# Kernel tuning notes

Measured on AMD Instinct MI355X. Metric: run time of the kernel, lower is better.

## Reference

```python
import jax, jax.numpy as jnp
import numpy as np

# dims: batch, tokens, model dim, heads, head_dim, context len, n_blocks, ffn dim
B, L, D, H, HD, S, NB, DFF = 1, 3072, 1024, 16, 64, 512, 2, 4096
T3, H3, W3 = 12, 16, 16  # latent video grid, T3*H3*W3 == L


def _ln(x):
    # LayerNorm, elementwise_affine=False, eps=1e-6
    m = jnp.mean(x, axis=-1, keepdims=True)
    v = jnp.mean(jnp.square(x - m), axis=-1, keepdims=True)
    return (x - m) * jax.lax.rsqrt(v + 1e-6)


def _rot_half(x):
    x1, x2 = jnp.split(x, 2, axis=-1)
    return jnp.concatenate([-x2, x1], axis=-1)


def _rope3d(head_dim, t, h, w):
    d = head_dim // 6
    def band(n):
        freqs = 1.0 / 10000.0 ** (np.arange(0, 2 * d, 2, dtype=np.float32) / (2 * d))
        return np.outer(np.arange(n, dtype=np.float32), freqs)  # [n, d]
    te, he, we = band(t), band(h), band(w)
    rope = np.zeros((t, h, w, head_dim), dtype=np.float32)
    rope[:, :, :, :d] = te[:, None, None, :]
    rope[:, :, :, d:2 * d] = he[None, :, None, :]
    rope[:, :, :, 2 * d:3 * d] = we[None, None, :, :]
    return jnp.asarray(rope.reshape(t * h * w, head_dim))


def _forward(x, timestep_emb, context_emb, rope_emb, adaW, adab, sqW, skW, svW,
             soW, sob, cqW, ckW, cvW, coW, cob, f1W, f1b, f2W, f2b):
    Bv, Lv, Dv = x.shape
    hd = rope_emb.shape[-1]
    nh = Dv // hd
    scale = hd ** -0.5
    cos = jnp.cos(rope_emb)[None, None]  # [1,1,L,hd]
    sin = jnp.sin(rope_emb)[None, None]

    def heads(y):  # [B,N,D] -> [B,H,N,hd]
        return y.reshape(Bv, -1, nh, hd).transpose(0, 2, 1, 3)

    def merge(y):  # [B,H,L,hd] -> [B,L,D]
        return y.transpose(0, 2, 1, 3).reshape(Bv, Lv, Dv)

    for i in range(adaW.shape[0]):
        mods = timestep_emb @ adaW[i].T + adab[i]  # [B, 6D]
        sh_msa, sc_msa, g_msa, sh_mlp, sc_mlp, g_mlp = jnp.split(mods, 6, axis=-1)
        # --- AdaLN + self-attention with RoPE ---
        hx = _ln(x) * (1.0 + sc_msa[:, None, :]) + sh_msa[:, None, :]
        q, k, v = heads(hx @ sqW[i].T), heads(hx @ skW[i].T), heads(hx @ svW[i].T)
        q = q * cos + _rot_half(q) * sin
        k = k * cos + _rot_half(k) * sin
        a = jax.nn.softmax(jnp.einsum('bhld,bhmd->bhlm', q, k) * scale, axis=-1)
        o = merge(jnp.einsum('bhlm,bhmd->bhld', a, v))
        x = x + g_msa[:, None, :] * (o @ soW[i].T + sob[i])
        # --- cross-attention (no gate, no modulation) ---
        hx = _ln(x)
        q = heads(hx @ cqW[i].T)
        k = heads(context_emb @ ckW[i].T)
        v = heads(context_emb @ cvW[i].T)
        a = jax.nn.softmax(jnp.einsum('bhld,bhsd->bhls', q, k) * scale, axis=-1)
        o = merge(jnp.einsum('bhls,bhsd->bhld', a, v))
        x = x + (o @ coW[i].T + cob[i])
        # --- AdaLN + MLP (exact GELU) ---
        hx = _ln(x) * (1.0 + sc_mlp[:, None, :]) + sh_mlp[:, None, :]
        hx = jax.nn.gelu(hx @ f1W[i].T + f1b[i], approximate=False)
        x = x + g_mlp[:, None, :] * (hx @ f2W[i].T + f2b[i])
    return x


def setup_inputs() -> dict:
    ks = jax.random.split(jax.random.key(0), 20)
    s = 0.02
    return {
        'x': jax.random.normal(ks[0], (B, L, D), jnp.float32),
        'timestep_emb': jax.random.normal(ks[1], (B, D), jnp.float32),
        'context_emb': jax.random.normal(ks[2], (B, S, D), jnp.float32),
        'rope_emb': _rope3d(HD, T3, H3, W3),
        'adaW': jax.random.normal(ks[3], (NB, 6 * D, D), jnp.float32) * s,
        'adab': jnp.zeros((NB, 6 * D), jnp.float32),
        'sqW': jax.random.normal(ks[4], (NB, D, D), jnp.float32) * s,
        'skW': jax.random.normal(ks[5], (NB, D, D), jnp.float32) * s,
        'svW': jax.random.normal(ks[6], (NB, D, D), jnp.float32) * s,
        'soW': jax.random.normal(ks[7], (NB, D, D), jnp.float32) * s,
        'sob': jnp.zeros((NB, D), jnp.float32),
        'cqW': jax.random.normal(ks[8], (NB, D, D), jnp.float32) * s,
        'ckW': jax.random.normal(ks[9], (NB, D, D), jnp.float32) * s,
        'cvW': jax.random.normal(ks[10], (NB, D, D), jnp.float32) * s,
        'coW': jax.random.normal(ks[11], (NB, D, D), jnp.float32) * s,
        'cob': jnp.zeros((NB, D), jnp.float32),
        'f1W': jax.random.normal(ks[12], (NB, DFF, D), jnp.float32) * s,
        'f1b': jnp.zeros((NB, DFF), jnp.float32),
        'f2W': jax.random.normal(ks[13], (NB, D, DFF), jnp.float32) * s,
        'f2b': jnp.zeros((NB, D), jnp.float32),
    }


def reference(x, timestep_emb, context_emb, rope_emb, adaW, adab, sqW, skW, svW,
              soW, sob, cqW, ckW, cvW, coW, cob, f1W, f1b, f2W, f2b):
    return _forward(x, timestep_emb, context_emb, rope_emb, adaW, adab, sqW, skW,
                    svW, soW, sob, cqW, ckW, cvW, coW, cob, f1W, f1b, f2W, f2b)
```

## Files before the change

### kernel.cpp

```cpp
#include <hip/hip_runtime.h>
#include <math.h>

typedef __attribute__((ext_vector_type(8))) short bf16x8;
typedef __attribute__((ext_vector_type(4))) float f32x4;
typedef unsigned short u16;
typedef unsigned int u32;

#define DEV static __device__ __forceinline__

typedef __attribute__((address_space(3))) u32 lds_u32;
typedef const __attribute__((address_space(1))) u32 glb_u32;

DEV void gload16(const void* g, void* l){
  __builtin_amdgcn_global_load_lds((glb_u32*)g, (lds_u32*)l, 16, 0, 0);
}

DEV u16 f2bf(float f){
  u32 u = __builtin_bit_cast(u32, f);
  u32 r = (u + 0x7fffu + ((u >> 16) & 1u)) >> 16;
  return (u16)r;
}
DEV float bf2f(u16 h){
  u32 u = ((u32)h) << 16;
  return __builtin_bit_cast(float, u);
}
DEV u32 cvtpk(float a, float b){
  u32 r;
  asm("v_cvt_pk_bf16_f32 %0, %1, %2" : "=v"(r) : "v"(a), "v"(b));
  return r;
}
DEV float gelu_exact(float x){ return 0.5f*x*(1.f+erff(x*0.70710678118654752f)); }

#define QSCALE 0.18033688f

DEV void xcd_remap(int &bx, int &by){
  int gx = gridDim.x, gy = gridDim.y;
  int n = gx*gy;
  if ((n & 7) == 0){
    int id = by*gx + bx;
    int q = n >> 3;
    int sid = (id & 7)*q + (id >> 3);
    bx = sid % gx;
    by = sid / gx;
  }
}

__global__ __launch_bounds__(256) void k_copy_f32(const float* __restrict__ in, float* __restrict__ out, int n4){
  int i = blockIdx.x*256 + threadIdx.x;
  if (i < n4) ((float4*)out)[i] = ((const float4*)in)[i];
}

__global__ __launch_bounds__(256) void k_cvt_bf16(const float* __restrict__ in, u16* __restrict__ out, int n4){
  int i = blockIdx.x*256 + threadIdx.x;
  if (i < n4){
    float4 v = ((const float4*)in)[i];
    ushort4 o;
    o.x = f2bf(v.x); o.y = f2bf(v.y); o.z = f2bf(v.z); o.w = f2bf(v.w);
    ((ushort4*)out)[i] = o;
  }
}

struct CvtArgs { const float4* s[16]; ushort4* d[16]; };
__global__ __launch_bounds__(256) void k_cvt_all(CvtArgs a){
  int i = blockIdx.x*256 + threadIdx.x;
  int seg = i >> 19;
  int off = i & 0x7FFFF;
  float4 v = a.s[seg][off];
  ushort4 o;
  o.x = f2bf(v.x); o.y = f2bf(v.y); o.z = f2bf(v.z); o.w = f2bf(v.w);
  a.d[seg][off] = o;
}

__global__ __launch_bounds__(256) void k_trig(const float* __restrict__ rope,
    float2* __restrict__ ctq, float2* __restrict__ ctk){
  int i = blockIdx.x*256 + threadIdx.x;
  int d = i & 63;
  float a = rope[i];
  float c = cosf(a), s = sinf(a);
  float sg = (d < 32) ? -s : s;
  ctk[i] = make_float2(c, sg);
  ctq[i] = make_float2(c*QSCALE, sg*QSCALE);
}

__global__ __launch_bounds__(256) void k_ada(const float* __restrict__ te,
    const float* __restrict__ adaW, const float* __restrict__ adab,
    float* __restrict__ mods){
  int row = blockIdx.x*4 + (threadIdx.x>>6);
  int lane = threadIdx.x & 63;
  const float* wr = adaW + (size_t)row*1024;
  float s = 0.f;
  #pragma unroll
  for (int j=0; j<4; j++){
    int c = lane*4 + j*256;
    float4 a = *(const float4*)(te + c);
    float4 b = *(const float4*)(wr + c);
    s += a.x*b.x + a.y*b.y + a.z*b.z + a.w*b.w;
  }
  #pragma unroll
  for (int off=32; off; off>>=1) s += __shfl_down(s, off);
  if (!lane) mods[row] = s + adab[row];
}

__global__ __launch_bounds__(256) void k_ln_mod(const float* __restrict__ x,
    const float* __restrict__ sh, const float* __restrict__ sc,
    u16* __restrict__ out){
  int row = blockIdx.x, t = threadIdx.x;
  const float* xr = x + (size_t)row*1024;
  float4 v = ((const float4*)xr)[t];
  float s  = v.x+v.y+v.z+v.w;
  float sq = v.x*v.x+v.y*v.y+v.z*v.z+v.w*v.w;
  #pragma unroll
  for (int off=32; off; off>>=1){ s += __shfl_down(s,off); sq += __shfl_down(sq,off); }
  __shared__ float red[8];
  int w = t>>6, lane = t&63;
  if (!lane){ red[w] = s; red[4+w] = sq; }
  __syncthreads();
  s  = red[0]+red[1]+red[2]+red[3];
  sq = red[4]+red[5]+red[6]+red[7];
  float mean = s*(1.f/1024.f);
  float var  = sq*(1.f/1024.f) - mean*mean;
  float rst  = rsqrtf(var + 1e-6f);
  float vv[4] = {v.x, v.y, v.z, v.w};
  ushort4 o;
  u16 ob[4];
  #pragma unroll
  for (int j=0;j<4;j++){
    int col = t*4+j;
    float y = (vv[j]-mean)*rst;
    if (sh) y = y*(1.f + sc[col]) + sh[col];
    ob[j] = f2bf(y);
  }
  o.x=ob[0]; o.y=ob[1]; o.z=ob[2]; o.w=ob[3];
  *(ushort4*)(out + (size_t)row*1024 + t*4) = o;
}

__global__ __launch_bounds__(256) void k_rope(u16* __restrict__ q, u16* __restrict__ k,
    const float* __restrict__ rope){
  int idx = blockIdx.x*256 + threadIdx.x;
  int d = idx & 31;
  int h = (idx >> 5) & 15;
  int p = idx >> 9;
  const float* rr = rope + (size_t)p*64;
  float a0 = rr[d], a1 = rr[d+32];
  float c0 = cosf(a0), s0 = sinf(a0);
  float c1 = cosf(a1), s1 = sinf(a1);
  size_t o = (size_t)p*1024 + h*64 + d;
  float q0 = bf2f(q[o]), q1 = bf2f(q[o+32]);
  q[o]    = f2bf((q0*c0 - q1*s0)*QSCALE);
  q[o+32] = f2bf((q1*c1 + q0*s1)*QSCALE);
  float k0 = bf2f(k[o]), k1 = bf2f(k[o+32]);
  k[o]    = f2bf(k0*c0 - k1*s0);
  k[o+32] = f2bf(k1*c1 + k0*s1);
}

DEV void gemm_loop(const u16* __restrict__ X, const u16* __restrict__ W,
                   int bm, int bn, int ld, int lenK, u16* As, u16* Bs, f32x4 acc[4][4])
{
  int t = threadIdx.x;
  int w = t>>6, lane = t&63;
  int wr = (w>>1)*64, wc = (w&1)*64;
  int fr = lane&15, g = lane>>4;
  int arow = lane>>2, acol = (lane&3)*8;
  const u16* xp = X + (size_t)(bm + w*32 + arow)*ld + acol;
  const u16* wp = W + (size_t)(bn + w*32 + arow)*ld + acol;
  int nk = lenK >> 5;
  {
    u16* a = As + w*1024; u16* b = Bs + w*1024;
    gload16(xp, a);             gload16(xp + (size_t)16*ld, a + 512);
    gload16(wp, b);             gload16(wp + (size_t)16*ld, b + 512);
  }
  for (int kt = 0; kt < nk; ++kt){
    __syncthreads();
    int cur = kt & 1;
    if (kt + 1 < nk){
      int nb = cur ^ 1;
      int k0 = (kt+1) << 5;
      u16* a = As + nb*4096 + w*1024; u16* b = Bs + nb*4096 + w*1024;
      gload16(xp + k0, a);        gload16(xp + k0 + (size_t)16*ld, a + 512);
      gload16(wp + k0, b);        gload16(wp + k0 + (size_t)16*ld, b + 512);
    }
    const u16* ab = As + cur*4096;
    const u16* bb = Bs + cur*4096;
    bf16x8 a[4], b[4];
    #pragma unroll
    for (int i=0;i<4;i++) a[i] = *(const bf16x8*)(ab + (wr+i*16+fr)*32 + g*8);
    #pragma unroll
    for (int i=0;i<4;i++) b[i] = *(const bf16x8*)(bb + (wc+i*16+fr)*32 + g*8);
    __builtin_amdgcn_s_setprio(1);
    #pragma unroll
    for (int i=0;i<4;i++)
      #pragma unroll
      for (int j=0;j<4;j++)
        acc[i][j] = __builtin_amdgcn_mfma_f32_16x16x32_bf16(a[i], b[j], acc[i][j], 0, 0, 0);
    __builtin_amdgcn_s_setprio(0);
  }
}

template<int EPI>
__global__ __launch_bounds__(256) void k_gemm_bf16(
    const u16* __restrict__ X, const u16* __restrict__ W,
    const float* __restrict__ bias,
    u16* __restrict__ Yout,
    const float* __restrict__ resin, float* __restrict__ resout,
    const float* __restrict__ gate,
    int M, int N, int K)
{
  __shared__ __align__(16) u16 As[2*128*32];
  __shared__ __align__(16) u16 Bs[2*128*32];
  int bx = blockIdx.x, by = blockIdx.y;
  xcd_remap(bx, by);
  int bm = bx*128, bn = by*128;
  f32x4 acc[4][4] = {};
  gemm_loop(X, W, bm, bn, K, K, As, Bs, acc);
  int lane = threadIdx.x & 63, w = threadIdx.x>>6;
  int wr = (w>>1)*64, wc = (w&1)*64;
  int fr = lane&15, g = lane>>4;
  #pragma unroll
  for (int i=0;i<4;i++){
    #pragma unroll
    for (int j=0;j<4;j++){
      int col = bn + wc + j*16 + fr;
      float bv = bias ? bias[col] : 0.f;
      #pragma unroll
      for (int r=0;r<4;r++){
        int row = bm + wr + i*16 + g*4 + r;
        float y = acc[i][j][r] + bv;
        if (EPI == 1){
          Yout[(size_t)row*N + col] = f2bf(gelu_exact(y));
        } else if (EPI == 2){
          float gt = gate ? gate[col] : 1.f;
          resout[(size_t)row*N + col] = resin[(size_t)row*N + col] + gt*y;
        } else {
          Yout[(size_t)row*N + col] = f2bf(y*QSCALE);
        }
      }
    }
  }
}

__global__ __launch_bounds__(256) void k_gemm_part(
    const u16* __restrict__ X, const u16* __restrict__ W,
    float* __restrict__ pp, int M, int N, int K, int Ks)
{
  __shared__ __align__(16) u16 As[2*128*32];
  __shared__ __align__(16) u16 Bs[2*128*32];
  int bx = blockIdx.x, by = blockIdx.y;
  xcd_remap(bx, by);
  int s = blockIdx.z;
  int bm = bx*128, bn = by*128;
  f32x4 acc[4][4] = {};
  gemm_loop(X + (size_t)s*Ks, W + (size_t)s*Ks, bm, bn, K, Ks, As, Bs, acc);
  float* out = pp + (size_t)s*M*N;
  int lane = threadIdx.x & 63, w = threadIdx.x>>6;
  int wr = (w>>1)*64, wc = (w&1)*64;
  int fr = lane&15, g = lane>>4;
  #pragma unroll
  for (int i=0;i<4;i++)
    #pragma unroll
    for (int j=0;j<4;j++){
      int col = bn + wc + j*16 + fr;
      #pragma unroll
      for (int r=0;r<4;r++){
        int row = bm + wr + i*16 + g*4 + r;
        out[(size_t)row*N + col] = acc[i][j][r];
      }
    }
}

template<int EPI>
__global__ __launch_bounds__(256) void k_reduce(
    const float* __restrict__ pp, int S, const float* __restrict__ bias,
    const float* __restrict__ resin, float* __restrict__ resout,
    const float* __restrict__ gate, u16* __restrict__ Ybf,
    int MN, int N)
{
  int idx = blockIdx.x*256 + threadIdx.x;
  int base = idx*4;
  if (base >= MN) return;
  float4 s4 = *(const float4*)(pp + base);
  for (int s=1; s<S; ++s){
    float4 t4 = *(const float4*)(pp + (size_t)s*MN + base);
    s4.x += t4.x; s4.y += t4.y; s4.z += t4.z; s4.w += t4.w;
  }
  int col = base & (N-1);
  float b0=0,b1=0,b2=0,b3=0;
  if (bias){ b0=bias[col]; b1=bias[col+1]; b2=bias[col+2]; b3=bias[col+3]; }
  if (EPI == 2){
    float g0=1,g1=1,g2=1,g3=1;
    if (gate){ g0=gate[col]; g1=gate[col+1]; g2=gate[col+2]; g3=gate[col+3]; }
    float4 rv = *(const float4*)(resin + base);
    float4 o;
    o.x = rv.x + g0*(s4.x+b0);
    o.y = rv.y + g1*(s4.y+b1);
    o.z = rv.z + g2*(s4.z+b2);
    o.w = rv.w + g3*(s4.w+b3);
    *(float4*)(resout + base) = o;
  } else {
    ushort4 o;
    o.x = f2bf((s4.x+b0)*QSCALE);
    o.y = f2bf((s4.y+b1)*QSCALE);
    o.z = f2bf((s4.z+b2)*QSCALE);
    o.w = f2bf((s4.w+b3)*QSCALE);
    *(ushort4*)(Ybf + base) = o;
  }
}

template<int MOD>
__global__ __launch_bounds__(256) void k_reduce_ln(
    const float* __restrict__ pp, int S, const float* __restrict__ bias,
    const float* __restrict__ resin, float* __restrict__ resout,
    const float* __restrict__ gate,
    const float* __restrict__ sh, const float* __restrict__ sc,
    u16* __restrict__ hx)
{
  int row = blockIdx.x, t = threadIdx.x;
  size_t base = (size_t)row*1024 + t*4;
  const size_t MN = (size_t)3072*1024;
  float4 s4 = *(const float4*)(pp + base);
  for (int s=1; s<S; ++s){
    float4 t4 = *(const float4*)(pp + (size_t)s*MN + base);
    s4.x += t4.x; s4.y += t4.y; s4.z += t4.z; s4.w += t4.w;
  }
  int col = t*4;
  float b0=0,b1=0,b2=0,b3=0;
  if (bias){ b0=bias[col]; b1=bias[col+1]; b2=bias[col+2]; b3=bias[col+3]; }
  float g0=1,g1=1,g2=1,g3=1;
  if (gate){ g0=gate[col]; g1=gate[col+1]; g2=gate[col+2]; g3=gate[col+3]; }
  float4 rv = *(const float4*)(resin + base);
  float y[4];
  y[0] = rv.x + g0*(s4.x+b0);
  y[1] = rv.y + g1*(s4.y+b1);
  y[2] = rv.z + g2*(s4.z+b2);
  y[3] = rv.w + g3*(s4.w+b3);
  float4 ov; ov.x=y[0]; ov.y=y[1]; ov.z=y[2]; ov.w=y[3];
  *(float4*)(resout + base) = ov;
  float s  = y[0]+y[1]+y[2]+y[3];
  float sq = y[0]*y[0]+y[1]*y[1]+y[2]*y[2]+y[3]*y[3];
  #pragma unroll
  for (int off=32; off; off>>=1){ s += __shfl_down(s,off); sq += __shfl_down(sq,off); }
  __shared__ float red[8];
  int w = t>>6, lane = t&63;
  if (!lane){ red[w] = s; red[4+w] = sq; }
  __syncthreads();
  s  = red[0]+red[1]+red[2]+red[3];
  sq = red[4]+red[5]+red[6]+red[7];
  float mean = s*(1.f/1024.f);
  float var  = sq*(1.f/1024.f) - mean*mean;
  float rst  = rsqrtf(var + 1e-6f);
  ushort4 o;
  u16 ob[4];
  #pragma unroll
  for (int j=0;j<4;j++){
    float yy = (y[j]-mean)*rst;
    if (MOD) yy = yy*(1.f + sc[col+j]) + sh[col+j];
    ob[j] = f2bf(yy);
  }
  o.x=ob[0]; o.y=ob[1]; o.z=ob[2]; o.w=ob[3];
  *(ushort4*)(hx + base) = o;
}

template<int MODE>
__global__ __launch_bounds__(256) void k_qkv(
    const u16* __restrict__ X,
    const u16* __restrict__ W0, const u16* __restrict__ W1, const u16* __restrict__ W2,
    u16* __restrict__ Y0, u16* __restrict__ Y1, u16* __restrict__ VT,
    const float2* __restrict__ ctq, const float2* __restrict__ ctk,
    int M, int ldvt)
{
  __shared__ __align__(16) u16 As[2*128*32];
  __shared__ __align__(16) u16 Bs[2*128*32];
  int bx = blockIdx.x, by = blockIdx.y;
  xcd_remap(bx, by);
  int bm = bx*128, bn = by*128;
  int sel = bn >> 10;
  int bnl = bn & 1023;
  const u16* W = (sel==0 ? W0 : (sel==1 ? W1 : W2));
  f32x4 acc[4][4] = {};
  gemm_loop(X, W, bm, bnl, 1024, 1024, As, Bs, acc);
  int lane = threadIdx.x & 63, w = threadIdx.x>>6;
  int wr = (w>>1)*64, wc = (w&1)*64;
  int fr = lane&15, g = lane>>4;
  if (sel < 2){
    u16* Y = (sel==0) ? Y0 : Y1;
    const float2* ct = (sel==0) ? ctq : ctk;
    #pragma unroll
    for (int i=0;i<4;i++)
      #pragma unroll
      for (int j=0;j<4;j++){
        int col = bnl + wc + j*16 + fr;
        int d = j*16 + fr;
        #pragma unroll
        for (int r=0;r<4;r++){
          int row = bm + wr + i*16 + g*4 + r;
          float2 cs = ct[row*64 + d];
          float yv = acc[i][j][r]*cs.x + acc[i][j^2][r]*cs.y;
          Y[(size_t)row*1024 + col] = f2bf(yv);
        }
      }
  } else {
    #pragma unroll
    for (int i=0;i<4;i++)
      #pragma unroll
      for (int j=0;j<4;j++){
        int col = bnl + wc + j*16 + fr;
        int row0 = bm + wr + i*16 + g*4;
        uint2 pk;
        pk.x = cvtpk(acc[i][j][0], acc[i][j][1]);
        pk.y = cvtpk(acc[i][j][2], acc[i][j][3]);
        *(uint2*)(VT + (size_t)col*ldvt + row0) = pk;
      }
  }
}

__global__ __launch_bounds__(256) void k_kv64(
    const u16* __restrict__ X,
    const u16* __restrict__ Wk, const u16* __restrict__ Wv,
    u16* __restrict__ Kout, u16* __restrict__ VTout, int ldvt)
{
  __shared__ __align__(16) u16 As[2*64*32];
  __shared__ __align__(16) u16 Bs[2*64*32];
  int bx = blockIdx.x, by = blockIdx.y;
  xcd_remap(bx, by);
  int bm = bx*64;
  int sel = by >> 4;
  int bnl = (by & 15)*64;
  const u16* W = sel ? Wv : Wk;
  int t = threadIdx.x, w = t>>6, lane = t&63;
  int wr = (w>>1)*32, wc = (w&1)*32;
  int fr = lane&15, g = lane>>4;
  f32x4 acc[2][2] = {};
  int arow = lane>>2, acol = (lane&3)*8;
  const u16* xp = X + (size_t)(bm + w*16 + arow)*1024 + acol;
  const u16* wp = W + (size_t)(bnl + w*16 + arow)*1024 + acol;
  {
    gload16(xp, As + w*512);
    gload16(wp, Bs + w*512);
  }
  for (int kt = 0; kt < 32; ++kt){
    __syncthreads();
    int cur = kt & 1;
    if (kt + 1 < 32){
      int nb = cur ^ 1;
      int k0 = (kt+1) << 5;
      gload16(xp + k0, As + nb*2048 + w*512);
      gload16(wp + k0, Bs + nb*2048 + w*512);
    }
    const u16* ab = As + cur*2048;
    const u16* bb = Bs + cur*2048;
    bf16x8 a[2], b[2];
    #pragma unroll
    for (int i=0;i<2;i++) a[i] = *(const bf16x8*)(ab + (wr+i*16+fr)*32 + g*8);
    #pragma unroll
    for (int i=0;i<2;i++) b[i] = *(const bf16x8*)(bb + (wc+i*16+fr)*32 + g*8);
    __builtin_amdgcn_s_setprio(1);
    #pragma unroll
    for (int i=0;i<2;i++)
      #pragma unroll
      for (int j=0;j<2;j++)
        acc[i][j] = __builtin_amdgcn_mfma_f32_16x16x32_bf16(a[i], b[j], acc[i][j], 0, 0, 0);
    __builtin_amdgcn_s_setprio(0);
  }
  #pragma unroll
  for (int i=0;i<2;i++)
    #pragma unroll
    for (int j=0;j<2;j++){
      int col = bnl + wc + j*16 + fr;
      if (sel == 0){
        #pragma unroll
        for (int r=0;r<4;r++){
          int row = bm + wr + i*16 + g*4 + r;
          Kout[(size_t)row*1024 + col] = f2bf(acc[i][j][r]);
        }
      } else {
        int row0 = bm + wr + i*16 + g*4;
        uint2 pk;
        pk.x = cvtpk(acc[i][j][0], acc[i][j][1]);
        pk.y = cvtpk(acc[i][j][2], acc[i][j][3]);
        *(uint2*)(VTout + (size_t)col*ldvt + row0) = pk;
      }
    }
}

template<int EPI>
__global__ __launch_bounds__(256) void k_gemm_f32(
    const u16* __restrict__ X, const float* __restrict__ W,
    const float* __restrict__ bias,
    u16* __restrict__ Yout,
    const float* __restrict__ resin, float* __restrict__ resout,
    const float* __restrict__ gate,
    int M, int N, int K)
{
  __shared__ __align__(16) u16 As[128][32];
  __shared__ __align__(16) u16 Bs[128][40];
  int bx = blockIdx.x, by = blockIdx.y;
  xcd_remap(bx, by);
  int bm = bx*128, bn = by*128;
  int t = threadIdx.x;
  int w = t>>6, lane = t&63;
  int wr = (w>>1)*64, wc = (w&1)*64;
  int fr = lane&15, g = lane>>4;
  f32x4 acc[4][4] = {};
  int arow = lane>>2, acol = (lane&3)*8;
  int srow = t>>2, scol = (t&3)*8;
  for (int k0=0; k0<K; k0+=32){
    #pragma unroll
    for (int inst=0; inst<2; ++inst){
      int r = w*32 + inst*16 + arow;
      gload16(X + (size_t)(bm+r)*K + k0 + acol, &As[w*32+inst*16][0]);
    }
    #pragma unroll
    for (int it=0; it<2; ++it){
      const float* wp = W + (size_t)(bn+srow+it*64)*K + k0 + scol;
      float4 f0 = *(const float4*)(wp);
      float4 f1 = *(const float4*)(wp+4);
      uint4 bw;
      bw.x = (u32)f2bf(f0.x) | ((u32)f2bf(f0.y)<<16);
      bw.y = (u32)f2bf(f0.z) | ((u32)f2bf(f0.w)<<16);
      bw.z = (u32)f2bf(f1.x) | ((u32)f2bf(f1.y)<<16);
      bw.w = (u32)f2bf(f1.z) | ((u32)f2bf(f1.w)<<16);
      *(uint4*)&Bs[srow+it*64][scol] = bw;
    }
    __syncthreads();
    bf16x8 a[4], b[4];
    #pragma unroll
    for (int i=0;i<4;i++) a[i] = *(const bf16x8*)&As[wr+i*16+fr][g*8];
    #pragma unroll
    for (int i=0;i<4;i++) b[i] = *(const bf16x8*)&Bs[wc+i*16+fr][g*8];
    #pragma unroll
    for (int i=0;i<4;i++)
      #pragma unroll
      for (int j=0;j<4;j++)
        acc[i][j] = __builtin_amdgcn_mfma_f32_16x16x32_bf16(a[i], b[j], acc[i][j], 0, 0, 0);
    __syncthreads();
  }
  #pragma unroll
  for (int i=0;i<4;i++){
    #pragma unroll
    for (int j=0;j<4;j++){
      int col = bn + wc + j*16 + fr;
      float bv = bias ? bias[col] : 0.f;
      #pragma unroll
      for (int r=0;r<4;r++){
        int row = bm + wr + i*16 + g*4 + r;
        float y = acc[i][j][r] + bv;
        if (EPI == 0){
          Yout[(size_t)row*N + col] = f2bf(y);
        } else if (EPI == 1){
          Yout[(size_t)row*N + col] = f2bf(gelu_exact(y));
        } else if (EPI == 2){
          float gt = gate ? gate[col] : 1.f;
          resout[(size_t)row*N + col] = resin[(size_t)row*N + col] + gt*y;
        } else if (EPI == 3){
          Yout[(size_t)col*M + row] = f2bf(y);
        } else {
          Yout[(size_t)row*N + col] = f2bf(y*QSCALE);
        }
      }
    }
  }
}

__global__ __launch_bounds__(256) void k_flash(
    const u16* __restrict__ Q, const u16* __restrict__ Kb, const u16* __restrict__ VT,
    u16* __restrict__ O, int Lkv)
{
  __shared__ __align__(16) u16 Ks[2*64*64];
  __shared__ __align__(16) u16 Vs[2*64*64];
  __shared__ __align__(16) u16 Ps[4][16][72];
  int bx = blockIdx.x, by = blockIdx.y;
  xcd_remap(bx, by);
  int h = by;
  int q0 = bx*64;
  int t = threadIdx.x, w = t>>6, lane = t&63;
  int fr = lane&15, g = lane>>4;
  const u16* qrow = Q + (size_t)(q0 + w*16 + fr)*1024 + h*64;
  bf16x8 aq0 = *(const bf16x8*)(qrow + g*8);
  bf16x8 aq1 = *(const bf16x8*)(qrow + 32 + g*8);
  f32x4 accO[4] = {};
  float l = 0.f;
  int slot = lane & 7, rop = lane >> 3;
  const u16* kbase = Kb + (size_t)h*64;
  const u16* vbase = VT + (size_t)h*64*Lkv;
  int nt = Lkv >> 6;
  auto stage = [&](int tt){
    int buf = tt & 1;
    int k0 = tt << 6;
    #pragma unroll
    for (int inst=0; inst<2; ++inst){
      int row = w*16 + inst*8 + rop;
      int ss = slot ^ (row & 7);
      gload16(kbase + (size_t)(k0+row)*1024 + ss*8, Ks + buf*4096 + row*64);
      gload16(vbase + (size_t)row*Lkv + k0 + ss*8, Vs + buf*4096 + row*64);
    }
  };
  stage(0);
  bf16x8 vp0[4], vp1[4];
  for (int tt=0; tt<nt; ++tt){
    __syncthreads();
    int cur = tt & 1;
    const u16* kc = Ks + cur*4096;
    const u16* vc = Vs + cur*4096;
    bf16x8 vn0[4], vn1[4];
    #pragma unroll
    for (int nd=0; nd<4; nd++){
      int rowV = nd*16 + fr;
      vn0[nd] = *(const bf16x8*)(vc + rowV*64 + ((g  ) ^ (rowV&7))*8);
      vn1[nd] = *(const bf16x8*)(vc + rowV*64 + ((4+g) ^ (rowV&7))*8);
    }
    bf16x8 ap0, ap1;
    if (tt > 0){
      ap0 = *(const bf16x8*)&Ps[w][fr][g*8];
      ap1 = *(const bf16x8*)&Ps[w][fr][32 + g*8];
    }
    if (tt+1 < nt) stage(tt+1);
    f32x4 st[4] = {};
    __builtin_amdgcn_s_setprio(1);
    #pragma unroll
    for (int kb=0;kb<4;kb++){
      int rowK = kb*16 + fr;
      bf16x8 b0 = *(const bf16x8*)(kc + rowK*64 + ((g  ) ^ (rowK&7))*8);
      bf16x8 b1 = *(const bf16x8*)(kc + rowK*64 + ((4+g) ^ (rowK&7))*8);
      st[kb] = __builtin_amdgcn_mfma_f32_16x16x32_bf16(b0, aq0, st[kb], 0,0,0);
      st[kb] = __builtin_amdgcn_mfma_f32_16x16x32_bf16(b1, aq1, st[kb], 0,0,0);
    }
    if (tt > 0){
      #pragma unroll
      for (int nd=0; nd<4; nd++){
        accO[nd] = __builtin_amdgcn_mfma_f32_16x16x32_bf16(ap0, vp0[nd], accO[nd], 0,0,0);
        accO[nd] = __builtin_amdgcn_mfma_f32_16x16x32_bf16(ap1, vp1[nd], accO[nd], 0,0,0);
      }
    }
    __builtin_amdgcn_s_setprio(0);
    float ts = 0.f;
    u32 pk[8];
    #pragma unroll
    for (int kb=0;kb<4;kb++){
      float p0 = exp2f(st[kb][0]);
      float p1 = exp2f(st[kb][1]);
      float p2 = exp2f(st[kb][2]);
      float p3 = exp2f(st[kb][3]);
      ts += (p0+p1)+(p2+p3);
      pk[kb*2]   = cvtpk(p0,p1);
      pk[kb*2+1] = cvtpk(p2,p3);
    }
    ts += __shfl_xor(ts, 16);
    ts += __shfl_xor(ts, 32);
    l += ts;
    #pragma unroll
    for (int kb=0;kb<4;kb++){
      uint2 pv; pv.x = pk[kb*2]; pv.y = pk[kb*2+1];
      *(uint2*)&Ps[w][fr][kb*16 + g*4] = pv;
    }
    #pragma unroll
    for (int nd=0; nd<4; nd++){ vp0[nd] = vn0[nd]; vp1[nd] = vn1[nd]; }
  }
  {
    bf16x8 ap0 = *(const bf16x8*)&Ps[w][fr][g*8];
    bf16x8 ap1 = *(const bf16x8*)&Ps[w][fr][32 + g*8];
    #pragma unroll
    for (int nd=0; nd<4; nd++){
      accO[nd] = __builtin_amdgcn_mfma_f32_16x16x32_bf16(ap0, vp0[nd], accO[nd], 0,0,0);
      accO[nd] = __builtin_amdgcn_mfma_f32_16x16x32_bf16(ap1, vp1[nd], accO[nd], 0,0,0);
    }
  }
  float rl = 1.f / l;
  #pragma unroll
  for (int r=0;r<4;r++){
    float rlq = __shfl(rl, g*4+r);
    int row = q0 + w*16 + g*4 + r;
    #pragma unroll
    for (int nd=0; nd<4; nd++)
      O[(size_t)row*1024 + h*64 + nd*16 + fr] = f2bf(accO[nd][r] * rlq);
  }
}

extern "C" void kernel_launch(void* const* d_in, const int* in_sizes, int n_in,
                              void* d_out, int out_size, void* d_ws, size_t ws_size,
                              hipStream_t stream){
  const float* x_in = (const float*)d_in[0];
  const float* te   = (const float*)d_in[1];
  const float* ctx  = (const float*)d_in[2];
  const float* rope = (const float*)d_in[3];
  const float* adaW = (const float*)d_in[4];
  const float* adab = (const float*)d_in[5];
  const float* sqW  = (const float*)d_in[6];
  const float* skW  = (const float*)d_in[7];
  const float* svW  = (const float*)d_in[8];
  const float* soW  = (const float*)d_in[9];
  const float* sob  = (const float*)d_in[10];
  const float* cqW  = (const float*)d_in[11];
  const float* ckW  = (const float*)d_in[12];
  const float* cvW  = (const float*)d_in[13];
  const float* coW  = (const float*)d_in[14];
  const float* cob  = (const float*)d_in[15];
  const float* f1W  = (const float*)d_in[16];
  const float* f1b  = (const float*)d_in[17];
  const float* f2W  = (const float*)d_in[18];
  const float* f2b  = (const float*)d_in[19];
  float* x = (float*)d_out;

  char* p = (char*)d_ws;
  size_t used = 0;
  auto alloc = [&](size_t bytes){
    void* r = (void*)(p + used);
    used += (bytes + 255) & ~(size_t)255;
    return r;
  };
  u16* hx   = (u16*)alloc((size_t)3072*1024*2);
  u16* qb   = (u16*)alloc((size_t)3072*1024*2);
  u16* kb   = (u16*)alloc((size_t)3072*1024*2);
  u16* vt   = (u16*)alloc((size_t)1024*3072*2);
  u16* ob   = (u16*)alloc((size_t)3072*1024*2);
  u16* mid  = (u16*)alloc((size_t)3072*4096*2);
  u16* ctxb = (u16*)alloc((size_t)512*1024*2);
  float* mods = (float*)alloc((size_t)2*6144*4);
  float2* ctq = (float2*)alloc((size_t)3072*64*8);
  float2* ctk = (float2*)alloc((size_t)3072*64*8);
  size_t base_used = used;
  const size_t NW_SMALL = (size_t)2*1024*1024;
  const size_t NW_BIG   = (size_t)2*4096*1024;
  size_t wbytes = (8*NW_SMALL + 2*NW_BIG)*2;
  bool pre = (base_used + wbytes + 4096) <= ws_size;

  u16 *sqWb=nullptr,*skWb=nullptr,*svWb=nullptr,*soWb=nullptr,
      *cqWb=nullptr,*ckWb=nullptr,*cvWb=nullptr,*coWb=nullptr,
      *f1Wb=nullptr,*f2Wb=nullptr;
  if (pre){
    sqWb=(u16*)alloc(NW_SMALL*2); skWb=(u16*)alloc(NW_SMALL*2);
    svWb=(u16*)alloc(NW_SMALL*2); soWb=(u16*)alloc(NW_SMALL*2);
    cqWb=(u16*)alloc(NW_SMALL*2); ckWb=(u16*)alloc(NW_SMALL*2);
    cvWb=(u16*)alloc(NW_SMALL*2); coWb=(u16*)alloc(NW_SMALL*2);
    f1Wb=(u16*)alloc(NW_BIG*2);   f2Wb=(u16*)alloc(NW_BIG*2);
  }
  const size_t PPN = (size_t)4*3072*1024;
  float* pp = nullptr;
  bool splitok = pre && (used + PPN*4 + 4096) <= ws_size;
  if (splitok) pp = (float*)alloc(PPN*4);
  const int MN = 3072*1024;

  if (pre){
    CvtArgs ca;
    const float* smallW[8] = {sqW,skW,svW,soW,cqW,ckW,cvW,coW};
    u16* smallD[8] = {sqWb,skWb,svWb,soWb,cqWb,ckWb,cvWb,coWb};
    for (int s=0; s<8; ++s){ ca.s[s] = (const float4*)smallW[s]; ca.d[s] = (ushort4*)smallD[s]; }
    for (int qd=0; qd<4; ++qd){
      ca.s[8+qd]  = (const float4*)f1W + (size_t)qd*524288;
      ca.d[8+qd]  = (ushort4*)f1Wb + (size_t)qd*524288;
      ca.s[12+qd] = (const float4*)f2W + (size_t)qd*524288;
      ca.d[12+qd] = (ushort4*)f2Wb + (size_t)qd*524288;
    }
    k_cvt_all<<<32768, 256, 0, stream>>>(ca);
  }
  k_cvt_bf16<<<512, 256, 0, stream>>>(ctx, ctxb, 131072);
  k_ada<<<3072, 256, 0, stream>>>(te, adaW, adab, mods);
  k_trig<<<768, 256, 0, stream>>>(rope, ctq, ctk);
  if (!splitok) k_copy_f32<<<3072, 256, 0, stream>>>(x_in, x, 786432);

  for (int i=0; i<2; ++i){
    const float* mi  = mods + (size_t)i*6144;
    const float* mi2 = mods + 6144;
    size_t wo = (size_t)i*1024*1024;
    size_t wof = (size_t)i*4096*1024;
    if (i == 0 || !splitok)
      k_ln_mod<<<3072,256,0,stream>>>(i==0 ? x_in : x, mi+0, mi+1024, hx);
    if (pre){
      k_qkv<0><<<dim3(24,24),256,0,stream>>>(hx, sqWb+wo, skWb+wo, svWb+wo, qb, kb, vt, ctq, ctk, 3072, 3072);
    } else {
      k_gemm_f32<0><<<dim3(24,8),256,0,stream>>>(hx, sqW+wo, nullptr, qb, nullptr,nullptr,nullptr, 3072,1024,1024);
      k_gemm_f32<0><<<dim3(24,8),256,0,stream>>>(hx, skW+wo, nullptr, kb, nullptr,nullptr,nullptr, 3072,1024,1024);
      k_gemm_f32<3><<<dim3(24,8),256,0,stream>>>(hx, svW+wo, nullptr, vt, nullptr,nullptr,nullptr, 3072,1024,1024);
      k_rope<<<6144,256,0,stream>>>(qb, kb, rope);
    }
    k_flash<<<dim3(48,16),256,0,stream>>>(qb, kb, vt, ob, 3072);
    if (splitok){
      k_gemm_part<<<dim3(24,8,2),256,0,stream>>>(ob, soWb+wo, pp, 3072,1024,1024,512);
      k_reduce_ln<0><<<3072,256,0,stream>>>(pp, 2, sob+(size_t)i*1024,
          (i==0 ? x_in : (const float*)x), x, mi+2048, nullptr, nullptr, hx);
    } else if (pre){
      k_gemm_bf16<2><<<dim3(24,8),256,0,stream>>>(ob, soWb+wo, sob+(size_t)i*1024, nullptr, x, x, mi+2048, 3072,1024,1024);
      k_ln_mod<<<3072,256,0,stream>>>(x, nullptr, nullptr, hx);
    } else {
      k_gemm_f32<2><<<dim3(24,8),256,0,stream>>>(ob, soW+wo, sob+(size_t)i*1024, nullptr, x, x, mi+2048, 3072,1024,1024);
      k_ln_mod<<<3072,256,0,stream>>>(x, nullptr, nullptr, hx);
    }
    if (splitok){
      k_gemm_part<<<dim3(24,8,2),256,0,stream>>>(hx, cqWb+wo, pp, 3072,1024,1024,512);
      k_reduce<4><<<3072,256,0,stream>>>(pp, 2, nullptr, nullptr, nullptr, nullptr, qb, MN, 1024);
      k_kv64<<<dim3(8,32),256,0,stream>>>(ctxb, ckWb+wo, cvWb+wo, kb, vt, 512);
    } else if (pre){
      k_gemm_bf16<4><<<dim3(24,8),256,0,stream>>>(hx, cqWb+wo, nullptr, qb, nullptr,nullptr,nullptr, 3072,1024,1024);
      k_kv64<<<dim3(8,32),256,0,stream>>>(ctxb, ckWb+wo, cvWb+wo, kb, vt, 512);
    } else {
      k_gemm_f32<4><<<dim3(24,8),256,0,stream>>>(hx, cqW+wo, nullptr, qb, nullptr,nullptr,nullptr, 3072,1024,1024);
      k_gemm_f32<0><<<dim3(4,8),256,0,stream>>>(ctxb, ckW+wo, nullptr, kb, nullptr,nullptr,nullptr, 512,1024,1024);
      k_gemm_f32<3><<<dim3(4,8),256,0,stream>>>(ctxb, cvW+wo, nullptr, vt, nullptr,nullptr,nullptr, 512,1024,1024);
    }
    k_flash<<<dim3(48,16),256,0,stream>>>(qb, kb, vt, ob, 512);
    if (splitok){
      k_gemm_part<<<dim3(24,8,2),256,0,stream>>>(ob, coWb+wo, pp, 3072,1024,1024,512);
      k_reduce_ln<1><<<3072,256,0,stream>>>(pp, 2, cob+(size_t)i*1024, x, x, nullptr, mi+3072, mi+4096, hx);
    } else if (pre){
      k_gemm_bf16<2><<<dim3(24,8),256,0,stream>>>(ob, coWb+wo, cob+(size_t)i*1024, nullptr, x, x, nullptr, 3072,1024,1024);
      k_ln_mod<<<3072,256,0,stream>>>(x, mi+3072, mi+4096, hx);
    } else {
      k_gemm_f32<2><<<dim3(24,8),256,0,stream>>>(ob, coW+wo, cob+(size_t)i*1024, nullptr, x, x, nullptr, 3072,1024,1024);
      k_ln_mod<<<3072,256,0,stream>>>(x, mi+3072, mi+4096, hx);
    }
    if (pre){
      k_gemm_bf16<1><<<dim3(24,32),256,0,stream>>>(hx, f1Wb+wof, f1b+(size_t)i*4096, mid, nullptr,nullptr,nullptr, 3072,4096,1024);
    } else {
      k_gemm_f32<1><<<dim3(24,32),256,0,stream>>>(hx, f1W+wof, f1b+(size_t)i*4096, mid, nullptr,nullptr,nullptr, 3072,4096,1024);
    }
    if (splitok){
      k_gemm_part<<<dim3(24,8,4),256,0,stream>>>(mid, f2Wb+wof, pp, 3072,1024,4096,1024);
      if (i == 0)
        k_reduce_ln<1><<<3072,256,0,stream>>>(pp, 4, f2b, x, x, mi+5120, mi2+0, mi2+1024, hx);
      else
        k_reduce<2><<<3072,256,0,stream>>>(pp, 4, f2b+1024, x, x, mi+5120, nullptr, MN, 1024);
    } else if (pre){
      k_gemm_bf16<2><<<dim3(24,8),256,0,stream>>>(mid, f2Wb+wof, f2b+(size_t)i*1024, nullptr, x, x, mi+5120, 3072,1024,4096);
    } else {
      k_gemm_f32<2><<<dim3(24,8),256,0,stream>>>(mid, f2W+wof, f2b+(size_t)i*1024, nullptr, x, x, mi+5120, 3072,1024,4096);
    }
  }
}
```

Before: 788.8 us.

## Load V fragments directly from global in flash kernel; raise split-K to 4

The flash attention kernel stops staging V tiles through LDS. Each wave now reads its V fragments straight from global memory every tile, and the P·V MFMA runs in the same iteration instead of being deferred one step. This removes LDS traffic and the software pipeline for V, but exposes global load latency and adds redundant global reads of V across waves. Separately, the split-K GEMMs for the 1024-deep projections go from 2 to 4 partitions, which adds parallelism at the cost of more partial-sum traffic in the reduce kernels.

```diff
diff --git a/kernel.cpp b/kernel.cpp
--- a/kernel.cpp
+++ b/kernel.cpp
@@ -565,7 +565,6 @@
     u16* __restrict__ O, int Lkv)
 {
   __shared__ __align__(16) u16 Ks[2*64*64];
-  __shared__ __align__(16) u16 Vs[2*64*64];
   __shared__ __align__(16) u16 Ps[4][16][72];
   int bx = blockIdx.x, by = blockIdx.y;
   xcd_remap(bx, by);
@@ -590,27 +589,20 @@
       int row = w*16 + inst*8 + rop;
       int ss = slot ^ (row & 7);
       gload16(kbase + (size_t)(k0+row)*1024 + ss*8, Ks + buf*4096 + row*64);
-      gload16(vbase + (size_t)row*Lkv + k0 + ss*8, Vs + buf*4096 + row*64);
     }
   };
   stage(0);
-  bf16x8 vp0[4], vp1[4];
   for (int tt=0; tt<nt; ++tt){
     __syncthreads();
     int cur = tt & 1;
     const u16* kc = Ks + cur*4096;
-    const u16* vc = Vs + cur*4096;
-    bf16x8 vn0[4], vn1[4];
+    int k0 = tt << 6;
+    bf16x8 vb0[4], vb1[4];
     #pragma unroll
     for (int nd=0; nd<4; nd++){
-      int rowV = nd*16 + fr;
-      vn0[nd] = *(const bf16x8*)(vc + rowV*64 + ((g  ) ^ (rowV&7))*8);
-      vn1[nd] = *(const bf16x8*)(vc + rowV*64 + ((4+g) ^ (rowV&7))*8);
-    }
-    bf16x8 ap0, ap1;
-    if (tt > 0){
-      ap0 = *(const bf16x8*)&Ps[w][fr][g*8];
-      ap1 = *(const bf16x8*)&Ps[w][fr][32 + g*8];
+      const u16* vrow = vbase + (size_t)(nd*16 + fr)*Lkv + k0;
+      vb0[nd] = *(const bf16x8*)(vrow + g*8);
+      vb1[nd] = *(const bf16x8*)(vrow + 32 + g*8);
     }
     if (tt+1 < nt) stage(tt+1);
     f32x4 st[4] = {};
@@ -622,13 +614,6 @@
       bf16x8 b1 = *(const bf16x8*)(kc + rowK*64 + ((4+g) ^ (rowK&7))*8);
       st[kb] = __builtin_amdgcn_mfma_f32_16x16x32_bf16(b0, aq0, st[kb], 0,0,0);
       st[kb] = __builtin_amdgcn_mfma_f32_16x16x32_bf16(b1, aq1, st[kb], 0,0,0);
-    }
-    if (tt > 0){
-      #pragma unroll
-      for (int nd=0; nd<4; nd++){
-        accO[nd] = __builtin_amdgcn_mfma_f32_16x16x32_bf16(ap0, vp0[nd], accO[nd], 0,0,0);
-        accO[nd] = __builtin_amdgcn_mfma_f32_16x16x32_bf16(ap1, vp1[nd], accO[nd], 0,0,0);
-      }
     }
     __builtin_amdgcn_s_setprio(0);
     float ts = 0.f;
@@ -651,17 +636,15 @@
       uint2 pv; pv.x = pk[kb*2]; pv.y = pk[kb*2+1];
       *(uint2*)&Ps[w][fr][kb*16 + g*4] = pv;
     }
-    #pragma unroll
-    for (int nd=0; nd<4; nd++){ vp0[nd] = vn0[nd]; vp1[nd] = vn1[nd]; }
-  }
-  {
     bf16x8 ap0 = *(const bf16x8*)&Ps[w][fr][g*8];
     bf16x8 ap1 = *(const bf16x8*)&Ps[w][fr][32 + g*8];
+    __builtin_amdgcn_s_setprio(1);
     #pragma unroll
     for (int nd=0; nd<4; nd++){
-      accO[nd] = __builtin_amdgcn_mfma_f32_16x16x32_bf16(ap0, vp0[nd], accO[nd], 0,0,0);
-      accO[nd] = __builtin_amdgcn_mfma_f32_16x16x32_bf16(ap1, vp1[nd], accO[nd], 0,0,0);
-    }
+      accO[nd] = __builtin_amdgcn_mfma_f32_16x16x32_bf16(ap0, vb0[nd], accO[nd], 0,0,0);
+      accO[nd] = __builtin_amdgcn_mfma_f32_16x16x32_bf16(ap1, vb1[nd], accO[nd], 0,0,0);
+    }
+    __builtin_amdgcn_s_setprio(0);
   }
   float rl = 1.f / l;
   #pragma unroll
@@ -773,8 +756,8 @@
     }
     k_flash<<<dim3(48,16),256,0,stream>>>(qb, kb, vt, ob, 3072);
     if (splitok){
-      k_gemm_part<<<dim3(24,8,2),256,0,stream>>>(ob, soWb+wo, pp, 3072,1024,1024,512);
-      k_reduce_ln<0><<<3072,256,0,stream>>>(pp, 2, sob+(size_t)i*1024,
+      k_gemm_part<<<dim3(24,8,4),256,0,stream>>>(ob, soWb+wo, pp, 3072,1024,1024,256);
+      k_reduce_ln<0><<<3072,256,0,stream>>>(pp, 4, sob+(size_t)i*1024,
           (i==0 ? x_in : (const float*)x), x, mi+2048, nullptr, nullptr, hx);
     } else if (pre){
       k_gemm_bf16<2><<<dim3(24,8),256,0,stream>>>(ob, soWb+wo, sob+(size_t)i*1024, nullptr, x, x, mi+2048, 3072,1024,1024);
@@ -784,8 +767,8 @@
       k_ln_mod<<<3072,256,0,stream>>>(x, nullptr, nullptr, hx);
     }
     if (splitok){
-      k_gemm_part<<<dim3(24,8,2),256,0,stream>>>(hx, cqWb+wo, pp, 3072,1024,1024,512);
-      k_reduce<4><<<3072,256,0,stream>>>(pp, 2, nullptr, nullptr, nullptr, nullptr, qb, MN, 1024);
+      k_gemm_part<<<dim3(24,8,4),256,0,stream>>>(hx, cqWb+wo, pp, 3072,1024,1024,256);
+      k_reduce<4><<<3072,256,0,stream>>>(pp, 4, nullptr, nullptr, nullptr, nullptr, qb, MN, 1024);
       k_kv64<<<dim3(8,32),256,0,stream>>>(ctxb, ckWb+wo, cvWb+wo, kb, vt, 512);
     } else if (pre){
       k_gemm_bf16<4><<<dim3(24,8),256,0,stream>>>(hx, cqWb+wo, nullptr, qb, nullptr,nullptr,nullptr, 3072,1024,1024);
@@ -797,8 +780,8 @@
     }
     k_flash<<<dim3(48,16),256,0,stream>>>(qb, kb, vt, ob, 512);
     if (splitok){
-      k_gemm_part<<<dim3(24,8,2),256,0,stream>>>(ob, coWb+wo, pp, 3072,1024,1024,512);
-      k_reduce_ln<1><<<3072,256,0,stream>>>(pp, 2, cob+(size_t)i*1024, x, x, nullptr, mi+3072, mi+4096, hx);
+      k_gemm_part<<<dim3(24,8,4),256,0,stream>>>(ob, coWb+wo, pp, 3072,1024,1024,256);
+      k_reduce_ln<1><<<3072,256,0,stream>>>(pp, 4, cob+(size_t)i*1024, x, x, nullptr, mi+3072, mi+4096, hx);
     } else if (pre){
       k_gemm_bf16<2><<<dim3(24,8),256,0,stream>>>(ob, coWb+wo, cob+(size_t)i*1024, nullptr, x, x, nullptr, 3072,1024,1024);
       k_ln_mod<<<3072,256,0,stream>>>(x, mi+3072, mi+4096, hx);
```

After: 945.5 us. 19.9% more time.
